# Kernel optimization log

Measured on AMD Instinct MI355X. Metric: run time of the kernel, lower is better.

The kernel has to match this reference:

```python
import jax, jax.numpy as jnp
import numpy as np

DEPTH = 2
DIM = 1024     # shot-embedding width
SDIM = 256     # SSM state width
B = 256        # batch (episodes x classes)
S = 64         # shots per class (scan length)
EPS = 1e-5


def setup_inputs() -> dict:
    key = jax.random.key(0)
    ks = jax.random.split(key, 10)
    sc = 0.02
    return {
        "shot_embeddings": jax.random.normal(ks[0], (B, S, DIM), jnp.float32),
        # per-layer selective-scan cell params (stacked over depth)
        "Wd": jax.random.normal(ks[1], (DEPTH, DIM, SDIM), jnp.float32) * sc,   # delta proj
        "bd": jnp.zeros((DEPTH, SDIM), jnp.float32),
        "Wi": jax.random.normal(ks[2], (DEPTH, DIM, SDIM), jnp.float32) * sc,   # input (B) proj
        "bi": jnp.zeros((DEPTH, SDIM), jnp.float32),
        "A_log": jax.random.normal(ks[3], (DEPTH, SDIM), jnp.float32),          # state decay param
        "Wo": jax.random.normal(ks[4], (DEPTH, SDIM, DIM), jnp.float32) * sc,   # readout (C) proj
        "bo": jnp.zeros((DEPTH, DIM), jnp.float32),
        # state_to_class Linear(state_dim, dim) per layer
        "Ws": jax.random.normal(ks[5], (DEPTH, SDIM, DIM), jnp.float32) * sc,
        "bs": jnp.zeros((DEPTH, DIM), jnp.float32),
        # LayerNorm
        "gamma": jnp.ones((DIM,), jnp.float32),
        "beta": jnp.zeros((DIM,), jnp.float32),
    }


def _run_selective_scan(x, Wd, bd, Wi, bi, A_log, Wo, bo):
    """Mamba-style selective scan over the shot axis.
    x: [B,S,D] -> (y: [B,S,D], final_state: [B,N])"""
    delta = jax.nn.softplus(jnp.einsum('bsd,dn->bsn', x, Wd) + bd)   # [B,S,N]
    u = jnp.einsum('bsd,dn->bsn', x, Wi) + bi                        # [B,S,N]
    decay = jnp.exp(-delta * jax.nn.softplus(A_log))                 # [B,S,N]
    drive = delta * u                                                # [B,S,N]

    def step(h, t):
        d, g = t
        h = d * h + g
        return h, h

    h0 = jnp.zeros((x.shape[0], Wd.shape[1]), x.dtype)
    final, hs = jax.lax.scan(step, h0, (decay.swapaxes(0, 1), drive.swapaxes(0, 1)))
    hs = hs.swapaxes(0, 1)                                           # [B,S,N]
    y = jnp.einsum('bsn,nd->bsd', hs, Wo) + bo                       # [B,S,D]
    return y, final


def reference(shot_embeddings, Wd, bd, Wi, bi, A_log, Wo, bo, Ws, bs, gamma, beta):
    hidden = shot_embeddings
    class_state = None
    for l in range(Wd.shape[0]):  # fixed small depth
        hidden, state = _run_selective_scan(hidden, Wd[l], bd[l], Wi[l], bi[l],
                                            A_log[l], Wo[l], bo[l])
        class_state = jnp.einsum('bn,nd->bd', state, Ws[l]) + bs[l]   # [B,D]
        hidden = hidden + class_state[:, None, :]
    pooled = class_state + hidden.mean(axis=1)                        # [B,D]
    mu = pooled.mean(axis=-1, keepdims=True)
    var = pooled.var(axis=-1, keepdims=True)
    class_repr = (pooled - mu) / jnp.sqrt(var + EPS) * gamma + beta
    return class_repr, hidden
```

## Files before the change

kernel.cpp:

```cpp
#include <hip/hip_runtime.h>
#include <hip/hip_bf16.h>

#define DEPTH 2
#define DIM   1024
#define SDIM  256
#define BATCH 256
#define SHOTS 64
#define M_TOT (BATCH*SHOTS)
#define SGRP  4
#define GSTEP (SHOTS/SGRP)

typedef __attribute__((ext_vector_type(8))) short bf16x8;
typedef __attribute__((ext_vector_type(4))) float f32x4;
typedef unsigned short u16;

__device__ __forceinline__ u16 f2bf(float f) {
    union { float f; unsigned u; } v; v.f = f;
    unsigned r = v.u + 0x7fffu + ((v.u >> 16) & 1u);
    return (u16)(r >> 16);
}

__device__ __forceinline__ unsigned pk_bf2(float a, float b) {
    union { __hip_bfloat162 h2; unsigned u; } c;
    c.h2 = __float22bfloat162_rn(make_float2(a, b));
    return c.u;
}

__device__ __forceinline__ float bf2f(u16 h) {
    union { unsigned u; float f; } c; c.u = (unsigned)h << 16; return c.f;
}

__device__ __forceinline__ float softplus_f(float x) {
    if (x > 15.f) return x;
    return __logf(1.f + __expf(x));
}

__device__ __forceinline__ void gld16(const u16* g, u16* l) {
    __builtin_amdgcn_global_load_lds(
        (const __attribute__((address_space(1))) unsigned int*)g,
        (__attribute__((address_space(3))) unsigned int*)l, 16, 0, 0);
}

__device__ __forceinline__ void transpose_body(
    float T[64][65], const float* __restrict__ A1, const float* __restrict__ A2,
    u16* __restrict__ out, int K, int N, int SPLIT, int k0, int n0, int layer,
    int tid)
{
    const bool first = (n0 < SPLIT);
    const int scols = first ? SPLIT : (N - SPLIT);
    const float* S = (first ? A1 : A2) + (size_t)layer * K * scols
                     + (first ? n0 : (n0 - SPLIT));
    out += (size_t)layer * K * N;

    #pragma unroll
    for (int i = 0; i < 4; ++i) {
        const int c = tid + i * 256;
        const int kr = c >> 4, cc = c & 15;
        const float4 v = *(const float4*)(S + (size_t)(k0 + kr) * scols + cc * 4);
        T[kr][cc * 4 + 0] = v.x; T[kr][cc * 4 + 1] = v.y;
        T[kr][cc * 4 + 2] = v.z; T[kr][cc * 4 + 3] = v.w;
    }
    __syncthreads();
    #pragma unroll
    for (int i = 0; i < 4; ++i) {
        const int c = tid + i * 256;
        const int nr = c >> 4, cc = c & 15;
        ushort4 h;
        h.x = f2bf(T[cc * 4 + 0][nr]); h.y = f2bf(T[cc * 4 + 1][nr]);
        h.z = f2bf(T[cc * 4 + 2][nr]); h.w = f2bf(T[cc * 4 + 3][nr]);
        *(ushort4*)&out[(size_t)(n0 + nr) * K + k0 + cc * 4] = h;
    }
}

__global__ __launch_bounds__(256)
void prep(const float* __restrict__ Wd, const float* __restrict__ Wi,
          const float* __restrict__ Wo, const float* __restrict__ Ws,
          const float* __restrict__ X0,
          u16* __restrict__ WcombT, u16* __restrict__ WoT,
          u16* __restrict__ Wsb, u16* __restrict__ Xbf)
{
    __shared__ float T[64][65];
    const int bid = blockIdx.x;
    const int tid = threadIdx.x;

    if (bid < 256) {
        const int kx = bid & 15, ny = (bid >> 4) & 7, lz = bid >> 7;
        transpose_body(T, Wd, Wi, WcombT, 1024, 512, 256, kx * 64, ny * 64, lz, tid);
    } else if (bid < 384) {
        const int sub = bid - 256;
        const int kx = sub & 3, ny = (sub >> 2) & 15, lz = sub >> 6;
        transpose_body(T, Wo, Wo, WoT, 256, 1024, 1024, kx * 64, ny * 64, lz, tid);
    } else if (bid < 640) {
        const size_t i = ((size_t)(bid - 384) * 256 + tid) * 8;
        const float4 a = *(const float4*)(Ws + i);
        const float4 b = *(const float4*)(Ws + i + 4);
        int4 o;
        o.x = (int)pk_bf2(a.x, a.y); o.y = (int)pk_bf2(a.z, a.w);
        o.z = (int)pk_bf2(b.x, b.y); o.w = (int)pk_bf2(b.z, b.w);
        *(int4*)(Wsb + i) = o;
    } else {
        const size_t total = (size_t)M_TOT * DIM;
        const size_t stride = (size_t)2048 * 256 * 8;
        for (size_t i = ((size_t)(bid - 640) * 256 + tid) * 8; i < total; i += stride) {
            const float4 a = *(const float4*)(X0 + i);
            const float4 b = *(const float4*)(X0 + i + 4);
            int4 o;
            o.x = (int)pk_bf2(a.x, a.y); o.y = (int)pk_bf2(a.z, a.w);
            o.z = (int)pk_bf2(b.x, b.y); o.w = (int)pk_bf2(b.z, b.w);
            *(int4*)(Xbf + i) = o;
        }
    }
}

#define BM 128
#define BN 128
#define BK 32

template<int EPI, bool SWIZ, bool BF16OUT, bool POOL>
__global__ __launch_bounds__(256)
void gemm_bf16(const u16* __restrict__ A, const u16* __restrict__ BT,
               void* __restrict__ Cv, const float* __restrict__ bo,
               const float* __restrict__ cs, float* __restrict__ pooled,
               int K, int ldc, int CB)
{
    __shared__ __align__(16) u16 As[BM * BK];
    __shared__ __align__(16) u16 Bs[BN * BK];

    const int tid = threadIdx.x;
    const int id  = blockIdx.x;
    int rb, cb;
    if (SWIZ) {
        const int xcd = id & 7, slot = id >> 3;
        rb = xcd + 8 * (slot / CB);
        cb = slot % CB;
    } else {
        rb = id / CB; cb = id % CB;
    }
    const int row0 = rb * BM, col0 = cb * BN;

    const int l  = tid & 63;
    const int w  = tid >> 6;
    const int wm = (w >> 1) * 64, wn = (w & 1) * 64;
    const int lr = l & 15, lq = l >> 4;

    const int sg   = w * 2;
    const int srow = l >> 2;
    const int scol = (l & 3) * 8;
    const u16* Ag = A  + (size_t)(row0 + sg * 16 + srow) * K + scol;
    const u16* Bg = BT + (size_t)(col0 + sg * 16 + srow) * K + scol;
    u16* Asd = &As[sg * 512 + l * 8];
    u16* Bsd = &Bs[sg * 512 + l * 8];

    f32x4 acc[4][4];
    #pragma unroll
    for (int i = 0; i < 4; ++i)
        #pragma unroll
        for (int j = 0; j < 4; ++j)
            acc[i][j] = (f32x4){0.f, 0.f, 0.f, 0.f};

    for (int k0 = 0; k0 < K; k0 += BK) {
        gld16(Ag + k0,                  Asd);
        gld16(Ag + (size_t)16 * K + k0, Asd + 512);
        gld16(Bg + k0,                  Bsd);
        gld16(Bg + (size_t)16 * K + k0, Bsd + 512);
        __syncthreads();

        bf16x8 af[4], bfr[4];
        #pragma unroll
        for (int i = 0; i < 4; ++i)
            af[i] = *(const bf16x8*)&As[(wm + i * 16 + lr) * BK + lq * 8];
        #pragma unroll
        for (int j = 0; j < 4; ++j)
            bfr[j] = *(const bf16x8*)&Bs[(wn + j * 16 + lr) * BK + lq * 8];

        #pragma unroll
        for (int i = 0; i < 4; ++i)
            #pragma unroll
            for (int j = 0; j < 4; ++j)
                acc[i][j] = __builtin_amdgcn_mfma_f32_16x16x32_bf16(
                    af[i], bfr[j], acc[i][j], 0, 0, 0);
        __syncthreads();
    }

    float psum[4] = {0.f, 0.f, 0.f, 0.f};
    #pragma unroll
    for (int i = 0; i < 4; ++i) {
        const int grow = row0 + wm + i * 16 + lq * 4;
        #pragma unroll
        for (int j = 0; j < 4; ++j) {
            const int gcol = col0 + wn + j * 16 + lr;
            float addv = 0.f;
            if (EPI >= 1) addv += bo[gcol];
            if (EPI == 2) addv += cs[(size_t)(grow >> 6) * DIM + gcol];
            #pragma unroll
            for (int r = 0; r < 4; ++r) {
                const float val = acc[i][j][r] + addv;
                if (BF16OUT) ((u16*)Cv)[(size_t)(grow + r) * ldc + gcol] = f2bf(val);
                else         ((float*)Cv)[(size_t)(grow + r) * ldc + gcol] = val;
                if (POOL) psum[j] += val;
            }
        }
    }
    if (POOL) {
        const int batch_w = (row0 + wm) >> 6;
        #pragma unroll
        for (int j = 0; j < 4; ++j) {
            float v = psum[j];
            v += __shfl_xor(v, 16, 64);
            v += __shfl_xor(v, 32, 64);
            if (lq == 0)
                pooled[(size_t)batch_w * DIM + col0 + wn + j * 16 + lr] = v;
        }
    }
}

__global__ __launch_bounds__(1024)
void scan_cs(const float* __restrict__ PQ,
             const float* __restrict__ bd, const float* __restrict__ bi,
             const float* __restrict__ A_log,
             const u16* __restrict__ Wsb, const float* __restrict__ bs,
             u16* __restrict__ hsb, float* __restrict__ csbuf)
{
    __shared__ __align__(16) float decS[GSTEP][1024];
    __shared__ float drvS[GSTEP][1024];
    __shared__ float2 grp[SGRP][SDIM];
    __shared__ float st[SDIM];

    const int tid = threadIdx.x;
    const int b = blockIdx.x;
    const int n = tid & 255;
    const int g = tid >> 8;
    const float bdv = bd[n], biv = bi[n];
    const float spA = softplus_f(A_log[n]);
    const size_t m0 = (size_t)b * SHOTS + g * GSTEP;
    const float* base = PQ + m0 * 512 + n;

    float a = 1.f, hl = 0.f;
    #pragma unroll
    for (int s = 0; s < GSTEP; ++s) {
        const float p = base[s * 512];
        const float q = base[s * 512 + SDIM];
        const float delta = softplus_f(p + bdv);
        const float d  = __expf(-delta * spA);
        const float gv = delta * (q + biv);
        decS[s][tid] = d; drvS[s][tid] = gv;
        a *= d; hl = d * hl + gv;
    }

    grp[g][n] = make_float2(a, hl);
    __syncthreads();

    float h = 0.f;
    for (int j = 0; j < g; ++j) {
        const float2 sv = grp[j][n];
        h = sv.x * h + sv.y;
    }

    u16* hout = hsb + m0 * SDIM + n;
    #pragma unroll
    for (int s = 0; s < GSTEP; ++s) {
        h = decS[s][tid] * h + drvS[s][tid];
        hout[s * SDIM] = f2bf(h);
    }
    if (g == SGRP - 1) st[n] = h;
    __syncthreads();

    const int dbase = n * 4;
    f32x4 part = {0.f, 0.f, 0.f, 0.f};
    const int kq = g * 64;
    #pragma unroll 8
    for (int k = 0; k < 64; ++k) {
        const float sk = st[kq + k];
        const ushort4 wv = *(const ushort4*)&Wsb[(size_t)(kq + k) * DIM + dbase];
        part[0] += sk * bf2f(wv.x); part[1] += sk * bf2f(wv.y);
        part[2] += sk * bf2f(wv.z); part[3] += sk * bf2f(wv.w);
    }
    f32x4* psum = (f32x4*)decS;
    psum[g * 256 + n] = part;
    __syncthreads();
    if (tid < 256) {
        const f32x4 s0 = psum[tid], s1 = psum[256 + tid];
        const f32x4 s2 = psum[512 + tid], s3 = psum[768 + tid];
        const float4 bv = *(const float4*)(bs + tid * 4);
        float4 o;
        o.x = bv.x + s0[0] + s1[0] + s2[0] + s3[0];
        o.y = bv.y + s0[1] + s1[1] + s2[1] + s3[1];
        o.z = bv.z + s0[2] + s1[2] + s2[2] + s3[2];
        o.w = bv.w + s0[3] + s1[3] + s2[3] + s3[3];
        *(float4*)(csbuf + (size_t)b * DIM + tid * 4) = o;
    }
}

__global__ __launch_bounds__(1024)
void final_kernel(const float* __restrict__ pooled, const float* __restrict__ cs,
                  const float* __restrict__ gamma, const float* __restrict__ beta,
                  float* __restrict__ out)
{
    const int b = blockIdx.x;
    const int d = threadIdx.x;

    const float p = cs[(size_t)b * DIM + d]
                  + pooled[(size_t)b * DIM + d] * (1.f / SHOTS);

    __shared__ float rsum[1024], rsq[1024];
    rsum[d] = p; rsq[d] = p * p;
    __syncthreads();
    for (int off = 512; off > 0; off >>= 1) {
        if (d < off) { rsum[d] += rsum[d + off]; rsq[d] += rsq[d + off]; }
        __syncthreads();
    }
    const float mu  = rsum[0] * (1.f / DIM);
    const float var = rsq[0] * (1.f / DIM) - mu * mu;
    const float inv = rsqrtf(var + 1e-5f);

    out[(size_t)b * DIM + d] = (p - mu) * inv * gamma[d] + beta[d];
}


extern "C" void kernel_launch(void* const* d_in, const int* in_sizes, int n_in,
                              void* d_out, int out_size, void* d_ws, size_t ws_size,
                              hipStream_t stream)
{
    const float* X0    = (const float*)d_in[0];
    const float* Wd    = (const float*)d_in[1];
    const float* bd    = (const float*)d_in[2];
    const float* Wi    = (const float*)d_in[3];
    const float* bi    = (const float*)d_in[4];
    const float* A_log = (const float*)d_in[5];
    const float* Wo    = (const float*)d_in[6];
    const float* bo    = (const float*)d_in[7];
    const float* Ws    = (const float*)d_in[8];
    const float* bs    = (const float*)d_in[9];
    const float* gamma = (const float*)d_in[10];
    const float* beta  = (const float*)d_in[11];

    float* out_cr     = (float*)d_out;
    float* out_hidden = out_cr + (size_t)BATCH * DIM;

    u16* Xbf = (u16*)out_hidden;

    char* w = (char*)d_ws;
    float*  PQ     = (float*)w;  w += (size_t)M_TOT * 512 * 4;
    float*  csbuf  = (float*)w;  w += (size_t)BATCH * DIM * 4;
    float*  pooled = (float*)w;  w += (size_t)BATCH * DIM * 4;
    u16*    hsb    = (u16*)w;    w += (size_t)M_TOT * SDIM * 2;
    u16*    WcombT = (u16*)w;    w += (size_t)DEPTH * 512 * 1024 * 2;
    u16*    WoT    = (u16*)w;    w += (size_t)DEPTH * 1024 * 256 * 2;
    u16*    Wsb    = (u16*)w;    w += (size_t)DEPTH * SDIM * DIM * 2;

    prep<<<2688, 256, 0, stream>>>(Wd, Wi, Wo, Ws, X0, WcombT, WoT, Wsb, Xbf);

    for (int l = 0; l < DEPTH; ++l) {
        gemm_bf16<0, true, false, false><<<512, 256, 0, stream>>>(
            Xbf, WcombT + (size_t)l * 512 * 1024, PQ, nullptr, nullptr, nullptr,
            1024, 512, 4);
        scan_cs<<<BATCH, 1024, 0, stream>>>(
            PQ, bd + l * SDIM, bi + l * SDIM, A_log + l * SDIM,
            Wsb + (size_t)l * SDIM * DIM, bs + l * DIM, hsb, csbuf);
        if (l < DEPTH - 1) {
            gemm_bf16<2, true, true, false><<<1024, 256, 0, stream>>>(
                hsb, WoT + (size_t)l * 1024 * 256, Xbf, bo + l * DIM, csbuf,
                nullptr, 256, 1024, 8);
        } else {
            gemm_bf16<2, true, false, true><<<1024, 256, 0, stream>>>(
                hsb, WoT + (size_t)l * 1024 * 256, out_hidden, bo + l * DIM, csbuf,
                pooled, 256, 1024, 8);
        }
    }
    final_kernel<<<BATCH, 1024, 0, stream>>>(pooled, csbuf, gamma, beta, out_cr);
}
```

Measured before the change: 272.3 us.

## Fuse selective scan into projection GEMM epilogue and class-state into readout GEMM

```diff
diff --git a/kernel.cpp b/kernel.cpp
--- a/kernel.cpp
+++ b/kernel.cpp
@@ -7,8 +7,6 @@
 #define BATCH 256
 #define SHOTS 64
 #define M_TOT (BATCH*SHOTS)
-#define SGRP  4
-#define GSTEP (SHOTS/SGRP)
 
 typedef __attribute__((ext_vector_type(8))) short bf16x8;
 typedef __attribute__((ext_vector_type(4))) float f32x4;
@@ -43,8 +41,8 @@
 
 __device__ __forceinline__ void transpose_body(
     float T[64][65], const float* __restrict__ A1, const float* __restrict__ A2,
-    u16* __restrict__ out, int K, int N, int SPLIT, int k0, int n0, int layer,
-    int tid)
+    u16* __restrict__ out, int K, int SPLIT, int k0, int n0, int destbase,
+    int layer, int N, int tid)
 {
     const bool first = (n0 < SPLIT);
     const int scols = first ? SPLIT : (N - SPLIT);
@@ -68,7 +66,7 @@
         ushort4 h;
         h.x = f2bf(T[cc * 4 + 0][nr]); h.y = f2bf(T[cc * 4 + 1][nr]);
         h.z = f2bf(T[cc * 4 + 2][nr]); h.w = f2bf(T[cc * 4 + 3][nr]);
-        *(ushort4*)&out[(size_t)(n0 + nr) * K + k0 + cc * 4] = h;
+        *(ushort4*)&out[(size_t)(destbase + nr) * K + k0 + cc * 4] = h;
     }
 }
 
@@ -85,11 +83,16 @@
 
     if (bid < 256) {
         const int kx = bid & 15, ny = (bid >> 4) & 7, lz = bid >> 7;
-        transpose_body(T, Wd, Wi, WcombT, 1024, 512, 256, kx * 64, ny * 64, lz, tid);
+        const int n0 = ny * 64;
+        const int destbase = (n0 < 256) ? (n0 >> 6) * 128
+                                        : ((n0 - 256) >> 6) * 128 + 64;
+        transpose_body(T, Wd, Wi, WcombT, 1024, 256, kx * 64, n0, destbase,
+                       lz, 512, tid);
     } else if (bid < 384) {
         const int sub = bid - 256;
         const int kx = sub & 3, ny = (sub >> 2) & 15, lz = sub >> 6;
-        transpose_body(T, Wo, Wo, WoT, 256, 1024, 1024, kx * 64, ny * 64, lz, tid);
+        transpose_body(T, Wo, Wo, WoT, 256, 1024, kx * 64, ny * 64, ny * 64,
+                       lz, 1024, tid);
     } else if (bid < 640) {
         const size_t i = ((size_t)(bid - 384) * 256 + tid) * 8;
         const float4 a = *(const float4*)(Ws + i);
@@ -116,27 +119,25 @@
 #define BN 128
 #define BK 32
 
-template<int EPI, bool SWIZ, bool BF16OUT, bool POOL>
+
 __global__ __launch_bounds__(256)
-void gemm_bf16(const u16* __restrict__ A, const u16* __restrict__ BT,
-               void* __restrict__ Cv, const float* __restrict__ bo,
-               const float* __restrict__ cs, float* __restrict__ pooled,
-               int K, int ldc, int CB)
+void gemm_pq_scan(const u16* __restrict__ A, const u16* __restrict__ BT,
+                  const float* __restrict__ bd, const float* __restrict__ bi,
+                  const float* __restrict__ A_log,
+                  u16* __restrict__ hsb, float* __restrict__ stateb, int CB)
 {
     __shared__ __align__(16) u16 As[BM * BK];
     __shared__ __align__(16) u16 Bs[BN * BK];
+    __shared__ float Ct[64][129];
+    __shared__ float2 grp[4][64];
 
     const int tid = threadIdx.x;
     const int id  = blockIdx.x;
-    int rb, cb;
-    if (SWIZ) {
-        const int xcd = id & 7, slot = id >> 3;
-        rb = xcd + 8 * (slot / CB);
-        cb = slot % CB;
-    } else {
-        rb = id / CB; cb = id % CB;
-    }
+    const int xcd = id & 7, slot = id >> 3;
+    const int rb = xcd + 8 * (slot / CB);
+    const int cb = slot % CB;
     const int row0 = rb * BM, col0 = cb * BN;
+    const int K = 1024;
 
     const int l  = tid & 63;
     const int w  = tid >> 6;
@@ -182,16 +183,166 @@
         __syncthreads();
     }
 
+    const int n0  = cb * 64;
+    const int seg = tid >> 6;
+    const int nl  = tid & 63;
+    const int n   = n0 + nl;
+    const float bdv = bd[n], biv = bi[n];
+    const float spA = softplus_f(A_log[n]);
+
+    for (int bl = 0; bl < 2; ++bl) {
+        if (bl) __syncthreads();
+        if ((w >> 1) == bl) {
+            #pragma unroll
+            for (int i = 0; i < 4; ++i)
+                #pragma unroll
+                for (int j = 0; j < 4; ++j)
+                    #pragma unroll
+                    for (int r = 0; r < 4; ++r)
+                        Ct[i * 16 + lq * 4 + r][wn + j * 16 + lr] = acc[i][j][r];
+        }
+        __syncthreads();
+
+        float a = 1.f, hl = 0.f;
+        #pragma unroll
+        for (int s2 = 0; s2 < 16; ++s2) {
+            const int s = seg * 16 + s2;
+            const float delta = softplus_f(Ct[s][nl] + bdv);
+            const float d  = __expf(-delta * spA);
+            const float gv = delta * (Ct[s][64 + nl] + biv);
+            Ct[s][nl] = d; Ct[s][64 + nl] = gv;
+            a *= d; hl = d * hl + gv;
+        }
+        grp[seg][nl] = make_float2(a, hl);
+        __syncthreads();
+
+        float h = 0.f;
+        for (int j = 0; j < seg; ++j) {
+            const float2 sv = grp[j][nl];
+            h = sv.x * h + sv.y;
+        }
+
+        const int b = 2 * rb + bl;
+        u16* hout = hsb + ((size_t)b * SHOTS + seg * 16) * SDIM + n;
+        #pragma unroll
+        for (int s2 = 0; s2 < 16; ++s2) {
+            const int s = seg * 16 + s2;
+            h = Ct[s][nl] * h + Ct[s][64 + nl];
+            hout[(size_t)s2 * SDIM] = f2bf(h);
+        }
+        if (seg == 3) stateb[(size_t)b * SDIM + n] = h;
+    }
+}
+
+template<bool BF16OUT, bool POOL>
+__global__ __launch_bounds__(256)
+void gemm_hidden(const u16* __restrict__ A, const u16* __restrict__ BT,
+                 void* __restrict__ Cv, const float* __restrict__ bo,
+                 const float* __restrict__ bs, const u16* __restrict__ Wsb,
+                 const float* __restrict__ stateb, float* __restrict__ pooled,
+                 float* __restrict__ csbuf, int CB)
+{
+    __shared__ __align__(16) u16 As[BM * BK];
+    __shared__ __align__(16) u16 Bs[BN * BK];
+    __shared__ float stL[512];
+    __shared__ float csL[2][128];
+
+    const int tid = threadIdx.x;
+    const int id  = blockIdx.x;
+    const int xcd = id & 7, slot = id >> 3;
+    const int rb = xcd + 8 * (slot / CB);
+    const int cb = slot % CB;
+    const int row0 = rb * BM, col0 = cb * BN;
+    const int K = 256, ldc = DIM;
+    const int b0 = row0 >> 6;
+
+    stL[tid]       = stateb[(size_t)b0 * SDIM + tid];
+    stL[tid + 256] = stateb[(size_t)b0 * SDIM + tid + 256];
+
+    const int l  = tid & 63;
+    const int w  = tid >> 6;
+    const int wm = (w >> 1) * 64, wn = (w & 1) * 64;
+    const int lr = l & 15, lq = l >> 4;
+
+    const int sg   = w * 2;
+    const int srow = l >> 2;
+    const int scol = (l & 3) * 8;
+    const u16* Ag = A  + (size_t)(row0 + sg * 16 + srow) * K + scol;
+    const u16* Bg = BT + (size_t)(col0 + sg * 16 + srow) * K + scol;
+    u16* Asd = &As[sg * 512 + l * 8];
+    u16* Bsd = &Bs[sg * 512 + l * 8];
+
+    f32x4 acc[4][4];
+    #pragma unroll
+    for (int i = 0; i < 4; ++i)
+        #pragma unroll
+        for (int j = 0; j < 4; ++j)
+            acc[i][j] = (f32x4){0.f, 0.f, 0.f, 0.f};
+
+    for (int k0 = 0; k0 < K; k0 += BK) {
+        gld16(Ag + k0,                  Asd);
+        gld16(Ag + (size_t)16 * K + k0, Asd + 512);
+        gld16(Bg + k0,                  Bsd);
+        gld16(Bg + (size_t)16 * K + k0, Bsd + 512);
+        __syncthreads();
+
+        bf16x8 af[4], bfr[4];
+        #pragma unroll
+        for (int i = 0; i < 4; ++i)
+            af[i] = *(const bf16x8*)&As[(wm + i * 16 + lr) * BK + lq * 8];
+        #pragma unroll
+        for (int j = 0; j < 4; ++j)
+            bfr[j] = *(const bf16x8*)&Bs[(wn + j * 16 + lr) * BK + lq * 8];
+
+        #pragma unroll
+        for (int i = 0; i < 4; ++i)
+            #pragma unroll
+            for (int j = 0; j < 4; ++j)
+                acc[i][j] = __builtin_amdgcn_mfma_f32_16x16x32_bf16(
+                    af[i], bfr[j], acc[i][j], 0, 0, 0);
+        __syncthreads();
+    }
+
+    {
+        const int kq = tid >> 6, blc = (tid >> 5) & 1, cg = tid & 31;
+        const int kb = kq * 64;
+        f32x4 part = {0.f, 0.f, 0.f, 0.f};
+        #pragma unroll 8
+        for (int k = 0; k < 64; ++k) {
+            const float sk = stL[blc * 256 + kb + k];
+            const ushort4 wv = *(const ushort4*)
+                &Wsb[(size_t)(kb + k) * DIM + col0 + cg * 4];
+            part[0] += sk * bf2f(wv.x); part[1] += sk * bf2f(wv.y);
+            part[2] += sk * bf2f(wv.z); part[3] += sk * bf2f(wv.w);
+        }
+        f32x4* psumL = (f32x4*)As;
+        psumL[tid] = part;
+        __syncthreads();
+        if (tid < 64) {
+            const int bl2 = tid >> 5, cg2 = tid & 31;
+            f32x4 s = psumL[bl2 * 32 + cg2];
+            #pragma unroll
+            for (int kq2 = 1; kq2 < 4; ++kq2)
+                s += psumL[kq2 * 64 + bl2 * 32 + cg2];
+            const float4 bv = *(const float4*)(bs + col0 + cg2 * 4);
+            float4 o;
+            o.x = s[0] + bv.x; o.y = s[1] + bv.y;
+            o.z = s[2] + bv.z; o.w = s[3] + bv.w;
+            *(float4*)&csL[bl2][cg2 * 4] = o;
+            *(float4*)(csbuf + (size_t)(b0 + bl2) * DIM + col0 + cg2 * 4) = o;
+        }
+        __syncthreads();
+    }
+
     float psum[4] = {0.f, 0.f, 0.f, 0.f};
     #pragma unroll
     for (int i = 0; i < 4; ++i) {
         const int grow = row0 + wm + i * 16 + lq * 4;
+        const int bl = (grow >> 6) & 1;
         #pragma unroll
         for (int j = 0; j < 4; ++j) {
             const int gcol = col0 + wn + j * 16 + lr;
-            float addv = 0.f;
-            if (EPI >= 1) addv += bo[gcol];
-            if (EPI == 2) addv += cs[(size_t)(grow >> 6) * DIM + gcol];
+            const float addv = bo[gcol] + csL[bl][gcol - col0];
             #pragma unroll
             for (int r = 0; r < 4; ++r) {
                 const float val = acc[i][j][r] + addv;
@@ -211,83 +362,6 @@
             if (lq == 0)
                 pooled[(size_t)batch_w * DIM + col0 + wn + j * 16 + lr] = v;
         }
-    }
-}
-
-__global__ __launch_bounds__(1024)
-void scan_cs(const float* __restrict__ PQ,
-             const float* __restrict__ bd, const float* __restrict__ bi,
-             const float* __restrict__ A_log,
-             const u16* __restrict__ Wsb, const float* __restrict__ bs,
-             u16* __restrict__ hsb, float* __restrict__ csbuf)
-{
-    __shared__ __align__(16) float decS[GSTEP][1024];
-    __shared__ float drvS[GSTEP][1024];
-    __shared__ float2 grp[SGRP][SDIM];
-    __shared__ float st[SDIM];
-
-    const int tid = threadIdx.x;
-    const int b = blockIdx.x;
-    const int n = tid & 255;
-    const int g = tid >> 8;
-    const float bdv = bd[n], biv = bi[n];
-    const float spA = softplus_f(A_log[n]);
-    const size_t m0 = (size_t)b * SHOTS + g * GSTEP;
-    const float* base = PQ + m0 * 512 + n;
-
-    float a = 1.f, hl = 0.f;
-    #pragma unroll
-    for (int s = 0; s < GSTEP; ++s) {
-        const float p = base[s * 512];
-        const float q = base[s * 512 + SDIM];
-        const float delta = softplus_f(p + bdv);
-        const float d  = __expf(-delta * spA);
-        const float gv = delta * (q + biv);
-        decS[s][tid] = d; drvS[s][tid] = gv;
-        a *= d; hl = d * hl + gv;
-    }
-
-    grp[g][n] = make_float2(a, hl);
-    __syncthreads();
-
-    float h = 0.f;
-    for (int j = 0; j < g; ++j) {
-        const float2 sv = grp[j][n];
-        h = sv.x * h + sv.y;
-    }
-
-    u16* hout = hsb + m0 * SDIM + n;
-    #pragma unroll
-    for (int s = 0; s < GSTEP; ++s) {
-        h = decS[s][tid] * h + drvS[s][tid];
-        hout[s * SDIM] = f2bf(h);
-    }
-    if (g == SGRP - 1) st[n] = h;
-    __syncthreads();
-
-    const int dbase = n * 4;
-    f32x4 part = {0.f, 0.f, 0.f, 0.f};
-    const int kq = g * 64;
-    #pragma unroll 8
-    for (int k = 0; k < 64; ++k) {
-        const float sk = st[kq + k];
-        const ushort4 wv = *(const ushort4*)&Wsb[(size_t)(kq + k) * DIM + dbase];
-        part[0] += sk * bf2f(wv.x); part[1] += sk * bf2f(wv.y);
-        part[2] += sk * bf2f(wv.z); part[3] += sk * bf2f(wv.w);
-    }
-    f32x4* psum = (f32x4*)decS;
-    psum[g * 256 + n] = part;
-    __syncthreads();
-    if (tid < 256) {
-        const f32x4 s0 = psum[tid], s1 = psum[256 + tid];
-        const f32x4 s2 = psum[512 + tid], s3 = psum[768 + tid];
-        const float4 bv = *(const float4*)(bs + tid * 4);
-        float4 o;
-        o.x = bv.x + s0[0] + s1[0] + s2[0] + s3[0];
-        o.y = bv.y + s0[1] + s1[1] + s2[1] + s3[1];
-        o.z = bv.z + s0[2] + s1[2] + s2[2] + s3[2];
-        o.w = bv.w + s0[3] + s1[3] + s2[3] + s3[3];
-        *(float4*)(csbuf + (size_t)b * DIM + tid * 4) = o;
     }
 }
 
@@ -340,9 +414,9 @@
     u16* Xbf = (u16*)out_hidden;
 
     char* w = (char*)d_ws;
-    float*  PQ     = (float*)w;  w += (size_t)M_TOT * 512 * 4;
     float*  csbuf  = (float*)w;  w += (size_t)BATCH * DIM * 4;
     float*  pooled = (float*)w;  w += (size_t)BATCH * DIM * 4;
+    float*  stateb = (float*)w;  w += (size_t)BATCH * SDIM * 4;
     u16*    hsb    = (u16*)w;    w += (size_t)M_TOT * SDIM * 2;
     u16*    WcombT = (u16*)w;    w += (size_t)DEPTH * 512 * 1024 * 2;
     u16*    WoT    = (u16*)w;    w += (size_t)DEPTH * 1024 * 256 * 2;
@@ -351,20 +425,20 @@
     prep<<<2688, 256, 0, stream>>>(Wd, Wi, Wo, Ws, X0, WcombT, WoT, Wsb, Xbf);
 
     for (int l = 0; l < DEPTH; ++l) {
-        gemm_bf16<0, true, false, false><<<512, 256, 0, stream>>>(
-            Xbf, WcombT + (size_t)l * 512 * 1024, PQ, nullptr, nullptr, nullptr,
-            1024, 512, 4);
-        scan_cs<<<BATCH, 1024, 0, stream>>>(
-            PQ, bd + l * SDIM, bi + l * SDIM, A_log + l * SDIM,
-            Wsb + (size_t)l * SDIM * DIM, bs + l * DIM, hsb, csbuf);
+        gemm_pq_scan<<<512, 256, 0, stream>>>(
+            Xbf, WcombT + (size_t)l * 512 * 1024,
+            bd + l * SDIM, bi + l * SDIM, A_log + l * SDIM,
+            hsb, stateb, 4);
         if (l < DEPTH - 1) {
-            gemm_bf16<2, true, true, false><<<1024, 256, 0, stream>>>(
-                hsb, WoT + (size_t)l * 1024 * 256, Xbf, bo + l * DIM, csbuf,
-                nullptr, 256, 1024, 8);
+            gemm_hidden<true, false><<<1024, 256, 0, stream>>>(
+                hsb, WoT + (size_t)l * 1024 * 256, Xbf, bo + l * DIM,
+                bs + l * DIM, Wsb + (size_t)l * SDIM * DIM, stateb,
+                nullptr, csbuf, 8);
         } else {
-            gemm_bf16<2, true, false, true><<<1024, 256, 0, stream>>>(
-                hsb, WoT + (size_t)l * 1024 * 256, out_hidden, bo + l * DIM, csbuf,
-                pooled, 256, 1024, 8);
+            gemm_hidden<false, true><<<1024, 256, 0, stream>>>(
+                hsb, WoT + (size_t)l * 1024 * 256, out_hidden, bo + l * DIM,
+                bs + l * DIM, Wsb + (size_t)l * SDIM * DIM, stateb,
+                pooled, csbuf, 8);
         }
     }
     final_kernel<<<BATCH, 1024, 0, stream>>>(pooled, csbuf, gamma, beta, out_cr);
```

New measurement: 252.4 us. -7.3%, faster.
